# Optimization experiments

Hardware: AMD Instinct MI355X
Metric: run time of the kernel (lower is better)

The kernel has to match this reference:

```python
import jax, jax.numpy as jnp
import numpy as np

NUM_HEADS = 8
D_MODEL = 512
D_Q = D_MODEL // NUM_HEADS
B, S = 4, 2048


def setup_inputs() -> dict:
    key = jax.random.key(0)
    ks = jax.random.split(key, 7)
    bound = 1.0 / np.sqrt(D_MODEL)  # kaiming_uniform with a=sqrt(5) on fan_in=d_model
    return {
        "x_query": jax.random.normal(ks[0], (B, S, D_MODEL), dtype=jnp.float32),
        "x_key": jax.random.normal(ks[1], (B, S, D_MODEL), dtype=jnp.float32),
        "x_value": jax.random.normal(ks[2], (B, S, D_MODEL), dtype=jnp.float32),
        "Q": jax.random.uniform(ks[3], (NUM_HEADS, D_MODEL, D_Q), minval=-bound, maxval=bound, dtype=jnp.float32),
        "K": jax.random.uniform(ks[4], (NUM_HEADS, D_MODEL, D_Q), minval=-bound, maxval=bound, dtype=jnp.float32),
        "V": jax.random.uniform(ks[5], (NUM_HEADS, D_MODEL, D_Q), minval=-bound, maxval=bound, dtype=jnp.float32),
        "Wout": jax.random.uniform(ks[6], (D_MODEL, D_MODEL), minval=-bound, maxval=bound, dtype=jnp.float32),
    }


def reference(x_query, x_key, x_value, Q, K, V, Wout):
    # per-head projections: [B,S,d_model] x [H,d_model,d_q] -> [B,H,S,d_q]
    q = jnp.einsum('bsd,hdq->bhsq', x_query, Q)
    k = jnp.einsum('bsd,hdq->bhsq', x_key, K)
    v = jnp.einsum('bsd,hdq->bhsq', x_value, V)
    scale = 1.0 / jnp.sqrt(jnp.asarray(q.shape[-1], q.dtype))
    scores = jnp.einsum('bhsq,bhtq->bhst', q, k) * scale  # [B,H,S,S]
    attn = jax.nn.softmax(scores, axis=-1)
    heads = jnp.einsum('bhst,bhtq->bhsq', attn, v)  # [B,H,S,d_q]
    # faithful to original: .view(B, S, -1) on [B,H,S,d_q] layout (no transpose)
    concat = heads.reshape(heads.shape[0], heads.shape[2], -1)
    return concat @ Wout.T
```

## Files before the change

### kernel.cpp

```cpp
#include <hip/hip_runtime.h>
#include <math.h>

#define BATCH 4
#define SEQ   2048
#define DM    512
#define NH    8
#define DQ    64
#define BS    (BATCH*SEQ)
#define BPAD  72
#define APAD  72

#define QSCALE 0.18033688011112042f

typedef short  short8   __attribute__((ext_vector_type(8)));
typedef float  floatx4  __attribute__((ext_vector_type(4)));
typedef float  floatx16 __attribute__((ext_vector_type(16)));
typedef unsigned short ushort8 __attribute__((ext_vector_type(8)));

__device__ __forceinline__ unsigned short f2bf(float f) {
    return (unsigned short)((__float_as_uint(f) + 0x8000u) >> 16);
}
__device__ __forceinline__ unsigned pack2bf(float a, float b) {
    unsigned ua = __float_as_uint(a) + 0x8000u;
    unsigned ub = __float_as_uint(b) + 0x8000u;
    return __builtin_amdgcn_perm(ub, ua, 0x07060302u);
}

__global__ __launch_bounds__(256) void convert_w_kernel(
    const float* __restrict__ Wq, const float* __restrict__ Wk,
    const float* __restrict__ Wv, const float* __restrict__ Wo,
    unsigned short* __restrict__ wt, unsigned short* __restrict__ wo)
{
    const int which = blockIdx.y;
    const int idx = blockIdx.x * 256 + threadIdx.x;
    if (which == 3) {
        float4 v = *(const float4*)(Wo + (size_t)idx * 4);
        uint2 o;
        o.x = pack2bf(v.x, v.y);
        o.y = pack2bf(v.z, v.w);
        *(uint2*)(wo + (size_t)idx * 4) = o;
    } else {
        const float* W = (which == 0) ? Wq : (which == 1) ? Wk : Wv;
        const int n   = idx >> 7;
        const int dd0 = (idx & 127) * 4;
        const int h = n >> 6, d = n & 63;
        uint2 o;
        o.x = pack2bf(W[((size_t)h * DM + dd0 + 0) * DQ + d],
                      W[((size_t)h * DM + dd0 + 1) * DQ + d]);
        o.y = pack2bf(W[((size_t)h * DM + dd0 + 2) * DQ + d],
                      W[((size_t)h * DM + dd0 + 3) * DQ + d]);
        *(uint2*)(wt + (size_t)which * (DM * DM) + (size_t)n * DM + dd0) = o;
    }
}

__global__ __launch_bounds__(256) void qkv_gemm_kernel(
    const float* __restrict__ Xq, const float* __restrict__ Xk,
    const float* __restrict__ Xv, const unsigned short* __restrict__ wt,
    unsigned short* __restrict__ Oq, unsigned short* __restrict__ Ok,
    unsigned short* __restrict__ Ovt)
{
    __shared__ unsigned short As[128][APAD];
    __shared__ unsigned short Bs[128][APAD];

    const int which = blockIdx.z;
    const float* X = (which == 0) ? Xq : (which == 1) ? Xk : Xv;
    const unsigned short* Bt = wt + (size_t)which * (DM * DM);

    const int m0 = blockIdx.x * 128;
    const int n0 = blockIdx.y * 128;
    const int t = threadIdx.x, w = t >> 6, lane = t & 63;
    const int quad = lane >> 4, qr = lane & 15;
    const int arow = t >> 4;
    const int acol = (t & 15) * 4;
    const int brow = t >> 3;
    const int bcol = (t & 7) * 8;
    const int mw = 64 * (w >> 1), nw = 64 * (w & 1);

    floatx4 acc[4][4] = {};
    float4  areg[8];
    ushort8 breg[4];

    #pragma unroll
    for (int i = 0; i < 8; ++i)
        areg[i] = *(const float4*)(X + (size_t)(m0 + i * 16 + arow) * DM + acol);
    #pragma unroll
    for (int i = 0; i < 4; ++i)
        breg[i] = *(const ushort8*)(Bt + (size_t)(n0 + i * 32 + brow) * DM + bcol);

    for (int k0 = 0; k0 < DM; k0 += 64) {
        __syncthreads();
        #pragma unroll
        for (int i = 0; i < 8; ++i) {
            uint2 o;
            o.x = pack2bf(areg[i].x, areg[i].y);
            o.y = pack2bf(areg[i].z, areg[i].w);
            *(uint2*)&As[i * 16 + arow][acol] = o;
        }
        #pragma unroll
        for (int i = 0; i < 4; ++i)
            *(ushort8*)&Bs[i * 32 + brow][bcol] = breg[i];
        __syncthreads();

        if (k0 + 64 < DM) {
            #pragma unroll
            for (int i = 0; i < 8; ++i)
                areg[i] = *(const float4*)(X + (size_t)(m0 + i * 16 + arow) * DM + k0 + 64 + acol);
            #pragma unroll
            for (int i = 0; i < 4; ++i)
                breg[i] = *(const ushort8*)(Bt + (size_t)(n0 + i * 32 + brow) * DM + k0 + 64 + bcol);
        }

        #pragma unroll
        for (int kh = 0; kh < 2; ++kh) {
            short8 af[4], bf[4];
            #pragma unroll
            for (int si = 0; si < 4; ++si)
                af[si] = *(const short8*)&As[mw + 16 * si + qr][kh * 32 + quad * 8];
            #pragma unroll
            for (int sj = 0; sj < 4; ++sj)
                bf[sj] = *(const short8*)&Bs[nw + 16 * sj + qr][kh * 32 + quad * 8];
            #pragma unroll
            for (int si = 0; si < 4; ++si)
                #pragma unroll
                for (int sj = 0; sj < 4; ++sj)
                    acc[si][sj] = __builtin_amdgcn_mfma_f32_16x16x32_bf16(
                        af[si], bf[sj], acc[si][sj], 0, 0, 0);
        }
    }

    const float osc = (which == 0) ? QSCALE : 1.0f;
    if (which < 2) {
        unsigned short* O = (which == 0) ? Oq : Ok;
        #pragma unroll
        for (int si = 0; si < 4; ++si) {
            #pragma unroll
            for (int sj = 0; sj < 4; ++sj) {
                const int col = n0 + nw + 16 * sj + qr;
                const int h = col >> 6, d = col & 63;
                #pragma unroll
                for (int r = 0; r < 4; ++r) {
                    const int row = m0 + mw + 16 * si + quad * 4 + r;
                    const int b = row >> 11, s = row & (SEQ - 1);
                    O[((size_t)(b * NH + h) * SEQ + s) * DQ + d] = f2bf(acc[si][sj][r] * osc);
                }
            }
        }
    } else {
        #pragma unroll
        for (int si = 0; si < 4; ++si) {
            #pragma unroll
            for (int sj = 0; sj < 4; ++sj) {
                const int col = n0 + nw + 16 * sj + qr;
                const int h = col >> 6, d = col & 63;
                #pragma unroll
                for (int r = 0; r < 4; ++r) {
                    const int row = m0 + mw + 16 * si + quad * 4 + r;
                    const int b = row >> 11, s = row & (SEQ - 1);
                    Ovt[((size_t)(b * NH + h) * DQ + d) * SEQ + s] = f2bf(acc[si][sj][r]);
                }
            }
        }
    }
}

__global__ __launch_bounds__(256) void out_gemm_kernel(
    const unsigned short* __restrict__ A, const unsigned short* __restrict__ Bt,
    float* __restrict__ C)
{
    __shared__ unsigned short As[64][APAD];
    __shared__ unsigned short Bs[128][APAD];

    const int m0 = blockIdx.x * 64;
    const int n0 = blockIdx.y * 128;
    const int t = threadIdx.x, w = t >> 6, lane = t & 63;
    const int quad = lane >> 4, qr = lane & 15;
    const int brow = t >> 3;
    const int bcol = (t & 7) * 8;
    const int mw = 32 * (w >> 1), nw = 64 * (w & 1);

    floatx4 acc[2][4] = {};
    ushort8 areg[2], breg[4];

    #pragma unroll
    for (int i = 0; i < 2; ++i)
        areg[i] = *(const ushort8*)(A + (size_t)(m0 + i * 32 + brow) * DM + bcol);
    #pragma unroll
    for (int i = 0; i < 4; ++i)
        breg[i] = *(const ushort8*)(Bt + (size_t)(n0 + i * 32 + brow) * DM + bcol);

    for (int k0 = 0; k0 < DM; k0 += 64) {
        __syncthreads();
        #pragma unroll
        for (int i = 0; i < 2; ++i)
            *(ushort8*)&As[i * 32 + brow][bcol] = areg[i];
        #pragma unroll
        for (int i = 0; i < 4; ++i)
            *(ushort8*)&Bs[i * 32 + brow][bcol] = breg[i];
        __syncthreads();

        if (k0 + 64 < DM) {
            #pragma unroll
            for (int i = 0; i < 2; ++i)
                areg[i] = *(const ushort8*)(A + (size_t)(m0 + i * 32 + brow) * DM + k0 + 64 + bcol);
            #pragma unroll
            for (int i = 0; i < 4; ++i)
                breg[i] = *(const ushort8*)(Bt + (size_t)(n0 + i * 32 + brow) * DM + k0 + 64 + bcol);
        }

        #pragma unroll
        for (int kh = 0; kh < 2; ++kh) {
            short8 af[2], bf[4];
            #pragma unroll
            for (int si = 0; si < 2; ++si)
                af[si] = *(const short8*)&As[mw + 16 * si + qr][kh * 32 + quad * 8];
            #pragma unroll
            for (int sj = 0; sj < 4; ++sj)
                bf[sj] = *(const short8*)&Bs[nw + 16 * sj + qr][kh * 32 + quad * 8];
            #pragma unroll
            for (int si = 0; si < 2; ++si)
                #pragma unroll
                for (int sj = 0; sj < 4; ++sj)
                    acc[si][sj] = __builtin_amdgcn_mfma_f32_16x16x32_bf16(
                        af[si], bf[sj], acc[si][sj], 0, 0, 0);
        }
    }

    #pragma unroll
    for (int si = 0; si < 2; ++si) {
        #pragma unroll
        for (int sj = 0; sj < 4; ++sj) {
            const int col = n0 + nw + 16 * sj + qr;
            #pragma unroll
            for (int r = 0; r < 4; ++r) {
                const int row = m0 + mw + 16 * si + quad * 4 + r;
                C[(size_t)row * DM + col] = acc[si][sj][r];
            }
        }
    }
}

__global__ __launch_bounds__(256, 4) void attn_kernel(
    const unsigned short* __restrict__ Qp, const unsigned short* __restrict__ Kp,
    const unsigned short* __restrict__ Vtp, unsigned short* __restrict__ Hd)
{
    __shared__ unsigned short smem[4 * 64 * BPAD];
    unsigned short (*Qs)[BPAD]  = (unsigned short (*)[BPAD])(smem);
    unsigned short (*Ks)[BPAD]  = (unsigned short (*)[BPAD])(smem + 64 * BPAD);
    unsigned short (*Vts)[BPAD] = (unsigned short (*)[BPAD])(smem + 2 * 64 * BPAD);
    unsigned short (*Ps)[BPAD]  = (unsigned short (*)[BPAD])(smem + 3 * 64 * BPAD);

    const int s0 = blockIdx.x * 64;
    const int h  = blockIdx.y;
    const int b  = blockIdx.z;
    const size_t bh    = (size_t)(b * NH + h);
    const size_t base  = bh * SEQ * DQ;
    const size_t vbase = bh * DQ * SEQ;

    const int t    = threadIdx.x;
    const int w    = t >> 6;
    const int lane = t & 63;
    const int qh   = w >> 1;
    const int kh   = w & 1;
    const int ln31 = lane & 31;
    const int lh   = lane >> 5;

    {
        const unsigned short* g = Qp + base + (size_t)s0 * DQ;
        #pragma unroll
        for (int i = 0; i < 2; ++i) {
            const int c = t + 256 * i;
            const int row = c >> 3, col8 = (c & 7) * 8;
            *(ushort8*)&Qs[row][col8] = *(const ushort8*)(g + row * DQ + col8);
        }
    }
    __syncthreads();
    short8 bq[4];
    #pragma unroll
    for (int s = 0; s < 4; ++s)
        bq[s] = *(const short8*)&Qs[32 * qh + ln31][16 * s + lh * 8];

    floatx16 accO[2] = {};
    float l_lane = 0.f;

    ushort8 kreg[2], vreg[2];
    {
        const unsigned short* gk = Kp + base;
        const unsigned short* gv = Vtp + vbase;
        #pragma unroll
        for (int i = 0; i < 2; ++i) {
            const int c = t + 256 * i;
            const int row = c >> 3, col8 = (c & 7) * 8;
            kreg[i] = *(const ushort8*)(gk + row * DQ + col8);
            vreg[i] = *(const ushort8*)(gv + (size_t)row * SEQ + col8);
        }
    }

    for (int kt = 0; kt < SEQ; kt += 64) {
        __syncthreads();
        #pragma unroll
        for (int i = 0; i < 2; ++i) {
            const int c = t + 256 * i;
            const int row = c >> 3, col8 = (c & 7) * 8;
            *(ushort8*)&Ks[row][col8]  = kreg[i];
            *(ushort8*)&Vts[row][col8] = vreg[i];
        }
        __syncthreads();

        if (kt + 64 < SEQ) {
            const unsigned short* gk = Kp + base + (size_t)(kt + 64) * DQ;
            const unsigned short* gv = Vtp + vbase + (kt + 64);
            #pragma unroll
            for (int i = 0; i < 2; ++i) {
                const int c = t + 256 * i;
                const int row = c >> 3, col8 = (c & 7) * 8;
                kreg[i] = *(const ushort8*)(gk + row * DQ + col8);
                vreg[i] = *(const ushort8*)(gv + (size_t)row * SEQ + col8);
            }
        }

        floatx16 z = {};
        #pragma unroll
        for (int s = 0; s < 4; ++s) {
            const short8 ak = *(const short8*)&Ks[32 * kh + ln31][16 * s + lh * 8];
            z = __builtin_amdgcn_mfma_f32_32x32x16_bf16(ak, bq[s], z, 0, 0, 0);
        }

        #pragma unroll
        for (int g = 0; g < 4; ++g) {
            const float p0 = __builtin_amdgcn_exp2f(z[4 * g + 0]);
            const float p1 = __builtin_amdgcn_exp2f(z[4 * g + 1]);
            const float p2 = __builtin_amdgcn_exp2f(z[4 * g + 2]);
            const float p3 = __builtin_amdgcn_exp2f(z[4 * g + 3]);
            l_lane += (p0 + p1) + (p2 + p3);
            uint2 pk;
            pk.x = pack2bf(p0, p1);
            pk.y = pack2bf(p2, p3);
            *(uint2*)&Ps[32 * qh + ln31][32 * kh + 8 * g + 4 * lh] = pk;
        }

        short8 ap[2];
        ap[0] = *(const short8*)&Ps[32 * qh + ln31][32 * kh + lh * 8];
        ap[1] = *(const short8*)&Ps[32 * qh + ln31][32 * kh + 16 + lh * 8];
        #pragma unroll
        for (int a = 0; a < 2; ++a) {
            #pragma unroll
            for (int s = 0; s < 2; ++s) {
                const short8 bv = *(const short8*)&Vts[32 * a + ln31][32 * kh + 16 * s + lh * 8];
                accO[a] = __builtin_amdgcn_mfma_f32_32x32x16_bf16(ap[s], bv, accO[a], 0, 0, 0);
            }
        }
    }

    float l2 = l_lane + __shfl_xor(l_lane, 32);
    float* Obuf = (float*)(smem + 64 * BPAD);
    float* lbuf = (float*)(smem + 3 * 64 * BPAD);
    __syncthreads();

    if (kh == 0) {
        if (lane < 32) lbuf[qh * 32 + lane] = l2;
        #pragma unroll
        for (int a = 0; a < 2; ++a)
            #pragma unroll
            for (int r = 0; r < 16; ++r) {
                const int qrow = (r & 3) + 8 * (r >> 2) + 4 * lh;
                Obuf[(32 * qh + qrow) * 66 + 32 * a + ln31] = accO[a][r];
            }
    }
    __syncthreads();

    if (kh == 1) {
        const float ltot = l2 + lbuf[qh * 32 + ln31];
        if (lane < 32) lbuf[64 + qh * 32 + lane] = 1.0f / ltot;
        #pragma unroll
        for (int a = 0; a < 2; ++a)
            #pragma unroll
            for (int r = 0; r < 16; ++r) {
                const int qrow = (r & 3) + 8 * (r >> 2) + 4 * lh;
                const float o = accO[a][r] + Obuf[(32 * qh + qrow) * 66 + 32 * a + ln31];
                const float iv = lbuf[64 + qh * 32 + qrow];
                Hd[base + (size_t)(s0 + 32 * qh + qrow) * DQ + 32 * a + ln31] = f2bf(o * iv);
            }
    }
}

extern "C" void kernel_launch(void* const* d_in, const int* in_sizes, int n_in,
                              void* d_out, int out_size, void* d_ws, size_t ws_size,
                              hipStream_t stream) {
    const float* xq = (const float*)d_in[0];
    const float* xk = (const float*)d_in[1];
    const float* xv = (const float*)d_in[2];
    const float* Qw = (const float*)d_in[3];
    const float* Kw = (const float*)d_in[4];
    const float* Vw = (const float*)d_in[5];
    const float* Wo = (const float*)d_in[6];
    float* out = (float*)d_out;

    unsigned short* ws = (unsigned short*)d_ws;
    unsigned short* wt    = ws;
    unsigned short* wo    = ws + (size_t)786432;
    unsigned short* q_ws  = ws + (size_t)1048576;
    unsigned short* k_ws  = ws + (size_t)5242880;
    unsigned short* vt_ws = ws + (size_t)9437184;
    unsigned short* h_ws  = ws + (size_t)13631488;

    convert_w_kernel<<<dim3(256, 4), 256, 0, stream>>>(Qw, Kw, Vw, Wo, wt, wo);
    qkv_gemm_kernel<<<dim3(64, 4, 3), 256, 0, stream>>>(xq, xk, xv, wt, q_ws, k_ws, vt_ws);
    attn_kernel<<<dim3(SEQ / 64, NH, BATCH), 256, 0, stream>>>(q_ws, k_ws, vt_ws, h_ws);
    out_gemm_kernel<<<dim3(128, 4), 256, 0, stream>>>(h_ws, wo, out);
}
```

Before: 192.0 us.

## Swizzle attention LDS tiles, pass P via permlane32 swap, remap blocks per XCD

Replaces the padded shared-memory tiles with XOR-swizzled unpadded tiles, which shrinks LDS use and allows launch bounds of 6 blocks per CU. The P tile no longer round-trips through LDS: packed bf16 probabilities are rearranged across half-waves with permlane32_swap to form the MFMA A operand directly. The grid becomes 1D, with (batch, head) pairs mapped so that each head's tiles stay on one XCD for L2 reuse of K and V. MFMA sections are wrapped in s_setprio. Risks include extra register pressure from the occupancy hint and the correctness of the lane permutation.

```diff
diff --git a/kernel.cpp b/kernel.cpp
--- a/kernel.cpp
+++ b/kernel.cpp
@@ -7,7 +7,6 @@
 #define NH    8
 #define DQ    64
 #define BS    (BATCH*SEQ)
-#define BPAD  72
 #define APAD  72
 
 #define QSCALE 0.18033688011112042f
@@ -16,6 +15,8 @@
 typedef float  floatx4  __attribute__((ext_vector_type(4)));
 typedef float  floatx16 __attribute__((ext_vector_type(16)));
 typedef unsigned short ushort8 __attribute__((ext_vector_type(8)));
+typedef unsigned uintx2 __attribute__((ext_vector_type(2)));
+typedef unsigned uintx4 __attribute__((ext_vector_type(4)));
 
 __device__ __forceinline__ unsigned short f2bf(float f) {
     return (unsigned short)((__float_as_uint(f) + 0x8000u) >> 16);
@@ -239,19 +240,23 @@
     }
 }
 
-__global__ __launch_bounds__(256, 4) void attn_kernel(
+__global__ __launch_bounds__(256, 6) void attn_kernel(
     const unsigned short* __restrict__ Qp, const unsigned short* __restrict__ Kp,
     const unsigned short* __restrict__ Vtp, unsigned short* __restrict__ Hd)
 {
-    __shared__ unsigned short smem[4 * 64 * BPAD];
-    unsigned short (*Qs)[BPAD]  = (unsigned short (*)[BPAD])(smem);
-    unsigned short (*Ks)[BPAD]  = (unsigned short (*)[BPAD])(smem + 64 * BPAD);
-    unsigned short (*Vts)[BPAD] = (unsigned short (*)[BPAD])(smem + 2 * 64 * BPAD);
-    unsigned short (*Ps)[BPAD]  = (unsigned short (*)[BPAD])(smem + 3 * 64 * BPAD);
-
-    const int s0 = blockIdx.x * 64;
-    const int h  = blockIdx.y;
-    const int b  = blockIdx.z;
+    __shared__ unsigned short smem[3 * 64 * 64];
+    unsigned short (*Qs)[64]  = (unsigned short (*)[64])(smem);
+    unsigned short (*Ks)[64]  = (unsigned short (*)[64])(smem + 64 * 64);
+    unsigned short (*Vts)[64] = (unsigned short (*)[64])(smem + 2 * 64 * 64);
+
+    const int f    = blockIdx.x;
+    const int xcd  = f & 7;
+    const int slot = f >> 3;
+    const int tile = slot & 31;
+    const int bhi  = (slot >> 5) * 8 + xcd;
+    const int b = bhi >> 3, h = bhi & 7;
+
+    const int s0 = tile * 64;
     const size_t bh    = (size_t)(b * NH + h);
     const size_t base  = bh * SEQ * DQ;
     const size_t vbase = bh * DQ * SEQ;
@@ -270,14 +275,17 @@
         for (int i = 0; i < 2; ++i) {
             const int c = t + 256 * i;
             const int row = c >> 3, col8 = (c & 7) * 8;
-            *(ushort8*)&Qs[row][col8] = *(const ushort8*)(g + row * DQ + col8);
+            *(ushort8*)&Qs[row][col8 ^ ((row & 7) * 8)] = *(const ushort8*)(g + row * DQ + col8);
         }
     }
     __syncthreads();
     short8 bq[4];
-    #pragma unroll
-    for (int s = 0; s < 4; ++s)
-        bq[s] = *(const short8*)&Qs[32 * qh + ln31][16 * s + lh * 8];
+    {
+        const int qrow = 32 * qh + ln31;
+        #pragma unroll
+        for (int s = 0; s < 4; ++s)
+            bq[s] = *(const short8*)&Qs[qrow][(16 * s + lh * 8) ^ ((qrow & 7) * 8)];
+    }
 
     floatx16 accO[2] = {};
     float l_lane = 0.f;
@@ -301,8 +309,9 @@
         for (int i = 0; i < 2; ++i) {
             const int c = t + 256 * i;
             const int row = c >> 3, col8 = (c & 7) * 8;
-            *(ushort8*)&Ks[row][col8]  = kreg[i];
-            *(ushort8*)&Vts[row][col8] = vreg[i];
+            const int sc = col8 ^ ((row & 7) * 8);
+            *(ushort8*)&Ks[row][sc]  = kreg[i];
+            *(ushort8*)&Vts[row][sc] = vreg[i];
         }
         __syncthreads();
 
@@ -319,12 +328,18 @@
         }
 
         floatx16 z = {};
-        #pragma unroll
-        for (int s = 0; s < 4; ++s) {
-            const short8 ak = *(const short8*)&Ks[32 * kh + ln31][16 * s + lh * 8];
-            z = __builtin_amdgcn_mfma_f32_32x32x16_bf16(ak, bq[s], z, 0, 0, 0);
-        }
-
+        __builtin_amdgcn_s_setprio(1);
+        {
+            const int krow = 32 * kh + ln31;
+            #pragma unroll
+            for (int s = 0; s < 4; ++s) {
+                const short8 ak = *(const short8*)&Ks[krow][(16 * s + lh * 8) ^ ((krow & 7) * 8)];
+                z = __builtin_amdgcn_mfma_f32_32x32x16_bf16(ak, bq[s], z, 0, 0, 0);
+            }
+        }
+        __builtin_amdgcn_s_setprio(0);
+
+        unsigned wg[4][2];
         #pragma unroll
         for (int g = 0; g < 4; ++g) {
             const float p0 = __builtin_amdgcn_exp2f(z[4 * g + 0]);
@@ -332,28 +347,37 @@
             const float p2 = __builtin_amdgcn_exp2f(z[4 * g + 2]);
             const float p3 = __builtin_amdgcn_exp2f(z[4 * g + 3]);
             l_lane += (p0 + p1) + (p2 + p3);
-            uint2 pk;
-            pk.x = pack2bf(p0, p1);
-            pk.y = pack2bf(p2, p3);
-            *(uint2*)&Ps[32 * qh + ln31][32 * kh + 8 * g + 4 * lh] = pk;
-        }
-
-        short8 ap[2];
-        ap[0] = *(const short8*)&Ps[32 * qh + ln31][32 * kh + lh * 8];
-        ap[1] = *(const short8*)&Ps[32 * qh + ln31][32 * kh + 16 + lh * 8];
+            wg[g][0] = pack2bf(p0, p1);
+            wg[g][1] = pack2bf(p2, p3);
+        }
+
+        const uintx2 e0 = __builtin_amdgcn_permlane32_swap(wg[0][0], wg[1][0], false, false);
+        const uintx2 e1 = __builtin_amdgcn_permlane32_swap(wg[0][1], wg[1][1], false, false);
+        const uintx2 e2 = __builtin_amdgcn_permlane32_swap(wg[2][0], wg[3][0], false, false);
+        const uintx2 e3 = __builtin_amdgcn_permlane32_swap(wg[2][1], wg[3][1], false, false);
+        uintx4 ua0, ua1;
+        ua0[0] = e0[0]; ua0[1] = e1[0]; ua0[2] = e0[1]; ua0[3] = e1[1];
+        ua1[0] = e2[0]; ua1[1] = e3[0]; ua1[2] = e2[1]; ua1[3] = e3[1];
+        const short8 ap0 = __builtin_bit_cast(short8, ua0);
+        const short8 ap1 = __builtin_bit_cast(short8, ua1);
+
+        __builtin_amdgcn_s_setprio(1);
         #pragma unroll
         for (int a = 0; a < 2; ++a) {
+            const int vrow = 32 * a + ln31;
             #pragma unroll
             for (int s = 0; s < 2; ++s) {
-                const short8 bv = *(const short8*)&Vts[32 * a + ln31][32 * kh + 16 * s + lh * 8];
-                accO[a] = __builtin_amdgcn_mfma_f32_32x32x16_bf16(ap[s], bv, accO[a], 0, 0, 0);
-            }
-        }
+                const short8 bv = *(const short8*)&Vts[vrow][(32 * kh + 16 * s + lh * 8) ^ ((vrow & 7) * 8)];
+                accO[a] = __builtin_amdgcn_mfma_f32_32x32x16_bf16(
+                    (s == 0) ? ap0 : ap1, bv, accO[a], 0, 0, 0);
+            }
+        }
+        __builtin_amdgcn_s_setprio(0);
     }
 
     float l2 = l_lane + __shfl_xor(l_lane, 32);
-    float* Obuf = (float*)(smem + 64 * BPAD);
-    float* lbuf = (float*)(smem + 3 * 64 * BPAD);
+    float* Obuf = (float*)smem;
+    float* lbuf = (float*)(smem + 3 * 64 * 64 - 256);
     __syncthreads();
 
     if (kh == 0) {
@@ -405,6 +429,6 @@
 
     convert_w_kernel<<<dim3(256, 4), 256, 0, stream>>>(Qw, Kw, Vw, Wo, wt, wo);
     qkv_gemm_kernel<<<dim3(64, 4, 3), 256, 0, stream>>>(xq, xk, xv, wt, q_ws, k_ws, vt_ws);
-    attn_kernel<<<dim3(SEQ / 64, NH, BATCH), 256, 0, stream>>>(q_ws, k_ws, vt_ws, h_ws);
+    attn_kernel<<<dim3(1024), 256, 0, stream>>>(q_ws, k_ws, vt_ws, h_ws);
     out_gemm_kernel<<<dim3(128, 4), 256, 0, stream>>>(h_ws, wo, out);
 }
```

After: 293.4 us. 1.53x slower.
